# Optimization experiments

Hardware: AMD Instinct MI355X
Metric: run time of the kernel (lower is better)

The kernel has to match this reference:

```python
import jax, jax.numpy as jnp
import numpy as np

HID, HQ, HKV, D, W = 2880, 64, 8, 64, 128  # hidden, q heads, kv heads, head_dim, sliding window
SCALE = D ** -0.5
NEG = -1e30


def _rope(x, cos, sin):
    # x: [B,S,H,D]; cos/sin: [S, D//2]
    c = cos[None, :, None, :].astype(x.dtype)
    s = sin[None, :, None, :].astype(x.dtype)
    x1, x2 = jnp.split(x, 2, axis=-1)
    return jnp.concatenate([x1 * c - x2 * s, x2 * c + x1 * s], axis=-1)


def setup_inputs() -> dict:
    key = jax.random.key(0)
    ks = jax.random.split(key, 12)
    B, S = 1, 4096
    std = 0.02
    x = jax.random.normal(ks[0], (B, S, HID), jnp.float32)
    # realistic rotary table (cos || sin), half-dim each
    inv_freq = 1.0 / (150000.0 ** (np.arange(0, D, 2, dtype=np.float32) / D))
    ang = np.arange(S, dtype=np.float32)[:, None] * inv_freq[None, :]
    freqs_cis = jnp.asarray(np.concatenate([np.cos(ang), np.sin(ang)], axis=-1), jnp.float32)  # [S, D]
    Wq = jax.random.normal(ks[1], (HID, HQ * D), jnp.float32) * std
    bq = jnp.zeros((HQ * D,), jnp.float32)
    Wk = jax.random.normal(ks[2], (HID, HKV * D), jnp.float32) * std
    bk = jnp.zeros((HKV * D,), jnp.float32)
    Wv = jax.random.normal(ks[3], (HID, HKV * D), jnp.float32) * std
    bv = jnp.zeros((HKV * D,), jnp.float32)
    Wo = jax.random.normal(ks[4], (HQ * D, HID), jnp.float32) * std
    bo = jnp.zeros((HID,), jnp.float32)
    sinks = jax.random.normal(ks[5], (HQ,), jnp.float32) * std
    return {"x": x, "freqs_cis": freqs_cis, "Wq": Wq, "bq": bq, "Wk": Wk, "bk": bk,
            "Wv": Wv, "bv": bv, "Wo": Wo, "bo": bo, "sinks": sinks}


def reference(x, freqs_cis, Wq, bq, Wk, bk, Wv, bv, Wo, bo, sinks):
    B, S, _ = x.shape
    G = HQ // HKV
    nb = S // W  # S must be a multiple of W
    cos, sin = jnp.split(freqs_cis, 2, axis=-1)

    q = (x @ Wq + bq).reshape(B, S, HQ, D)
    k = (x @ Wk + bk).reshape(B, S, HKV, D)
    v = (x @ Wv + bv).reshape(B, S, HKV, D)
    q = _rope(q, cos, sin)
    k = _rope(k, cos, sin)

    q = q.transpose(0, 2, 1, 3)  # [B,HQ,S,D]
    k = k.transpose(0, 2, 1, 3)  # [B,HKV,S,D]
    v = v.transpose(0, 2, 1, 3)

    # blocked sliding-window: each query block of size W sees keys [blk*W - W, blk*W + W)
    qb = q.reshape(B, HKV, G, nb, W, D)
    kp = jnp.pad(k, ((0, 0), (0, 0), (W, 0), (0, 0)))  # prepend W zero keys
    vp = jnp.pad(v, ((0, 0), (0, 0), (W, 0), (0, 0)))
    widx = jnp.arange(nb)[:, None] * W + jnp.arange(2 * W)[None, :]  # [nb, 2W]
    kb = kp[:, :, widx]  # [B,HKV,nb,2W,D]
    vb = vp[:, :, widx]

    scores = jnp.einsum('bkgntd,bkncd->bkgntc', qb, kb) * SCALE  # [B,HKV,G,nb,W,2W]

    t = jnp.arange(W)[:, None]
    j = jnp.arange(2 * W)[None, :]
    band = (j >= t + 1) & (j <= t + W)  # 0 <= qpos - kpos <= W-1
    kpos_ok = (jnp.arange(nb)[:, None] * W - W + jnp.arange(2 * W)[None, :]) >= 0  # [nb,2W]
    mask = band[None, :, :] & kpos_ok[:, None, :]  # [nb,W,2W]
    scores = jnp.where(mask[None, None, None], scores, NEG)

    sink = sinks.reshape(HKV, G)[None, :, :, None, None]  # [1,HKV,G,1,1]
    m = jnp.maximum(scores.max(axis=-1), sink)  # [B,HKV,G,nb,W]
    e = jnp.exp(scores - m[..., None])
    denom = e.sum(axis=-1) + jnp.exp(sink - m)
    p = e / denom[..., None]

    o = jnp.einsum('bkgntc,bkncd->bkgntd', p, vb)  # [B,HKV,G,nb,W,D]
    o = o.reshape(B, HQ, S, D).transpose(0, 2, 1, 3).reshape(B, S, HQ * D)
    return o @ Wo + bo
```

## Files before the change

### kernel.cpp

```cpp
#include <hip/hip_runtime.h>
#include <hip/hip_bf16.h>
#include <stdint.h>


typedef __attribute__((ext_vector_type(8))) short bf16x8;
typedef __attribute__((ext_vector_type(4))) float f32x4;
typedef __attribute__((ext_vector_type(8))) unsigned short ushort8;

#define DEVI static __device__ __forceinline__

DEVI unsigned short f2bf(float f) {
  unsigned x = __float_as_uint(f);
  return (unsigned short)((x + 0x7fffu + ((x >> 16) & 1u)) >> 16);
}
DEVI float bf2f(unsigned short u) { return __uint_as_float(((unsigned)u) << 16); }

DEVI void async16(const void* g, void* l) {
  __builtin_amdgcn_global_load_lds(
      (const __attribute__((address_space(1))) void*)g,
      (__attribute__((address_space(3))) void*)l, 16, 0, 0);
}

__global__ void k_cast_bf16(const float* __restrict__ src,
                            unsigned short* __restrict__ dst, long n) {
  long i = ((long)blockIdx.x * blockDim.x + threadIdx.x) * 4;
  const long stride = (long)gridDim.x * blockDim.x * 4;
  for (; i < n; i += stride) {
    float4 v = *(const float4*)(src + i);
    ushort4 o = make_ushort4(f2bf(v.x), f2bf(v.y), f2bf(v.z), f2bf(v.w));
    *(ushort4*)(dst + i) = o;
  }
}

__global__ void k_transpose_cast(const float* __restrict__ src,
                                 unsigned short* __restrict__ dst,
                                 int R, int C) {
  __shared__ float tile[64][65];
  const int t = threadIdx.x;
  const int r0 = blockIdx.y * 64, c0 = blockIdx.x * 64;
#pragma unroll
  for (int i = 0; i < 16; i++) {
    int r = i * 4 + (t >> 6), c = t & 63;
    float v = 0.f;
    if (c0 + c < C) v = src[(long)(r0 + r) * C + c0 + c];
    tile[r][c] = v;
  }
  __syncthreads();
#pragma unroll
  for (int i = 0; i < 16; i++) {
    int nn = i * 4 + (t >> 6), kk = t & 63;
    dst[(long)(c0 + nn) * R + r0 + kk] = f2bf(tile[kk][nn]);
  }
}

__global__ void k_concat_bias(const float* __restrict__ bq,
                              const float* __restrict__ bk,
                              const float* __restrict__ bv,
                              float* __restrict__ dst) {
  int i = blockIdx.x * 256 + threadIdx.x;
  if (i < 5120)
    dst[i] = (i < 4096) ? bq[i] : ((i < 4608) ? bk[i - 4096] : bv[i - 4608]);
}

#define STG(c, half, t)                                                        \
  do {                                                                         \
    const int tt_ = ((t) < NT) ? (t) : NT - 1;                                 \
    const long ko_ = (long)tt_ * 64;                                           \
    if ((half) < 2) {                                                          \
      const unsigned short* s_ = gA + (long)(half) * 128 * Kd + ko_;           \
      unsigned short* d_ = &As_[c][(((half) * 128) + w8) * 64];                \
      async16(s_, d_);                                                         \
      async16(s_ + 64 * (long)Kd, d_ + 64 * 64);                               \
    } else {                                                                   \
      const unsigned short* s_ = gB + (long)((half) - 2) * 128 * Kd + ko_;     \
      unsigned short* d_ = &Bs_[c][((((half) - 2) * 128) + w8) * 64];          \
      async16(s_, d_);                                                         \
      async16(s_ + 64 * (long)Kd, d_ + 64 * 64);                               \
    }                                                                          \
  } while (0)

#define LOADA(c, mh)                                                           \
  do {                                                                         \
    _Pragma("unroll") for (int m4 = 0; m4 < 4; m4++) {                         \
      const unsigned short* r_ =                                               \
          &As_[c][(wr128 + ((mh)*4 + m4) * 16 + ll) * 64];                     \
      aF[m4][0] = *(const bf16x8*)(r_ + sl0 * 8);                              \
      aF[m4][1] = *(const bf16x8*)(r_ + sl1 * 8);                              \
    }                                                                          \
  } while (0)

#define LOADB(c, nh)                                                           \
  do {                                                                         \
    _Pragma("unroll") for (int n2 = 0; n2 < 2; n2++) {                         \
      const unsigned short* r_ =                                               \
          &Bs_[c][(wc64 + ((nh)*2 + n2) * 16 + ll) * 64];                      \
      bF[nh][n2][0] = *(const bf16x8*)(r_ + sl0 * 8);                          \
      bF[nh][n2][1] = *(const bf16x8*)(r_ + sl1 * 8);                          \
    }                                                                          \
  } while (0)

#define MFMAQ(mh, nh)                                                          \
  do {                                                                         \
    __builtin_amdgcn_s_setprio(1);                                             \
    _Pragma("unroll") for (int m4 = 0; m4 < 4; m4++)                           \
        _Pragma("unroll") for (int n2 = 0; n2 < 2; n2++) {                     \
      acc[(mh)*4 + m4][(nh)*2 + n2] = __builtin_amdgcn_mfma_f32_16x16x32_bf16( \
          aF[m4][0], bF[nh][n2][0], acc[(mh)*4 + m4][(nh)*2 + n2], 0, 0, 0);   \
      acc[(mh)*4 + m4][(nh)*2 + n2] = __builtin_amdgcn_mfma_f32_16x16x32_bf16( \
          aF[m4][1], bF[nh][n2][1], acc[(mh)*4 + m4][(nh)*2 + n2], 0, 0, 0);   \
    }                                                                          \
    __builtin_amdgcn_s_setprio(0);                                             \
  } while (0)

#define BAR() __builtin_amdgcn_s_barrier()
#define VM2() asm volatile("s_waitcnt vmcnt(2)" ::: "memory")

template <bool OUT_BF16, bool NMASK>
__global__ __launch_bounds__(512, 2) void k_gemm8(
    const unsigned short* __restrict__ A, const unsigned short* __restrict__ Bt,
    const float* __restrict__ bias, void* __restrict__ Cout,
    int Kd, int NN, int ldc, int Nreal) {
  __shared__ unsigned short As_[2][256 * 64];
  __shared__ unsigned short Bs_[2][256 * 64];
  const int tid = threadIdx.x;
  const int w = tid >> 6, l = tid & 63;
  const int wr = w >> 2, wc = w & 3;
  const int lg = l >> 4, ll = l & 15;
  const int w8 = w * 8;
  const int wr128 = wr * 128, wc64 = wc * 64;
  const int sl0 = lg ^ (ll & 7), sl1 = sl0 ^ 4;
  const int NT = Kd >> 6;

  const int b = blockIdx.x;
  const int cpx = gridDim.x >> 3;
  const int tile = (b & 7) * cpx + (b >> 3);
  const int tm = tile / NN, tn = tile % NN;
  const long m0 = (long)tm * 256, n0 = (long)tn * 256;

  const unsigned short* gA =
      A + (m0 + (tid >> 3)) * (long)Kd + (((tid & 7) ^ ((tid >> 3) & 7)) << 3);
  const unsigned short* gB =
      Bt + (n0 + (tid >> 3)) * (long)Kd + (((tid & 7) ^ ((tid >> 3) & 7)) << 3);

  f32x4 acc[8][4];
#pragma unroll
  for (int i = 0; i < 8; i++)
#pragma unroll
    for (int j = 0; j < 4; j++) acc[i][j] = (f32x4){0.f, 0.f, 0.f, 0.f};
  bf16x8 aF[4][2], bF[2][2][2];

  STG(0, 0, 0); STG(0, 1, 0); STG(0, 2, 0); STG(0, 3, 0);
  STG(1, 0, 1);
  VM2();
  BAR();

  const int NITER = NT >> 1;
  for (int i = 0; i < NITER; i++) {
    const int t = 2 * i;
    LOADA(0, 0); LOADB(0, 0); STG(1, 1, t + 1); BAR(); MFMAQ(0, 0); BAR();
    LOADB(0, 1);              STG(1, 2, t + 1); BAR(); MFMAQ(0, 1); BAR();
    LOADA(0, 1);              STG(1, 3, t + 1); BAR(); MFMAQ(1, 1); BAR();
    STG(0, 0, t + 2); VM2();                    BAR(); MFMAQ(1, 0); BAR();
    LOADA(1, 0); LOADB(1, 0); STG(0, 1, t + 2); BAR(); MFMAQ(0, 0); BAR();
    LOADB(1, 1);              STG(0, 2, t + 2); BAR(); MFMAQ(0, 1); BAR();
    LOADA(1, 1);              STG(0, 3, t + 2); BAR(); MFMAQ(1, 1); BAR();
    STG(1, 0, t + 3); VM2();                    BAR(); MFMAQ(1, 0); BAR();
  }
  if (NT & 1) {
    LOADA(0, 0); LOADB(0, 0); MFMAQ(0, 0);
    LOADB(0, 1); MFMAQ(0, 1);
    LOADA(0, 1); MFMAQ(1, 1);
    MFMAQ(1, 0);
  }

#pragma unroll
  for (int nn = 0; nn < 4; nn++) {
    int col = (int)n0 + wc64 + nn * 16 + ll;
    bool ok = (!NMASK) || (col < Nreal);
    float bv_ = ok ? bias[col] : 0.f;
#pragma unroll
    for (int m = 0; m < 8; m++) {
      long row = m0 + wr128 + m * 16 + lg * 4;
#pragma unroll
      for (int j = 0; j < 4; j++) {
        float v = acc[m][nn][j] + bv_;
        if (ok) {
          if (OUT_BF16)
            ((unsigned short*)Cout)[(row + j) * (long)ldc + col] = f2bf(v);
          else
            ((float*)Cout)[(row + j) * (long)ldc + col] = v;
        }
      }
    }
  }
}

__global__ void k_rope(unsigned short* __restrict__ qkv,
                       const float* __restrict__ fc) {
  const int s = blockIdx.x;
  const float* f = fc + (long)s * 64;
  unsigned short* row = qkv + (long)s * 5120;
  for (int i = threadIdx.x; i < 72 * 32; i += 256) {
    int hh = i >> 5, d = i & 31;
    float c = f[d], sn = f[32 + d];
    int base = hh * 64 + d;
    float x1 = bf2f(row[base]), x2 = bf2f(row[base + 32]);
    row[base] = f2bf(x1 * c - x2 * sn);
    row[base + 32] = f2bf(x2 * c + x1 * sn);
  }
}

__global__ void k_transpose_v(const unsigned short* __restrict__ qkv,
                              unsigned short* __restrict__ vt) {
  __shared__ unsigned short tile[64][72];
  const int t = threadIdx.x;
  const int ts = blockIdx.x;
  const int tj = blockIdx.y;
#pragma unroll
  for (int i = 0; i < 2; i++) {
    int s = i * 32 + (t >> 3), j = (t & 7) * 8;
    *(ushort8*)&tile[s][j] =
        *(const ushort8*)(qkv + (long)(ts * 64 + s) * 5120 + 4608 + tj * 64 + j);
  }
  __syncthreads();
  int j = t >> 2, s0 = (t & 3) * 16;
  ushort8 v0, v1;
#pragma unroll
  for (int x = 0; x < 8; x++) {
    v0[x] = tile[s0 + x][j];
    v1[x] = tile[s0 + 8 + x][j];
  }
  unsigned short* dst = vt + (long)(tj * 64 + j) * 4096 + ts * 64 + s0;
  *(ushort8*)dst = v0;
  *(ushort8*)(dst + 8) = v1;
}

__global__ __launch_bounds__(256) void k_attn(
    const unsigned short* __restrict__ qkv, const unsigned short* __restrict__ vt,
    const float* __restrict__ sinks, unsigned short* __restrict__ o) {
  __shared__ unsigned short Ps[4][32][136];
  __shared__ unsigned short Ks[128][72];
  __shared__ unsigned short Vts[64][136];
  unsigned short(*Qs)[72] = (unsigned short(*)[72]) & Ps[0][0][0];

  const int n = blockIdx.x, h = blockIdx.y;
  const int kvh = h >> 3;
  const int t = threadIdx.x, w = t >> 6, l = t & 63;
  const int lg = l >> 4, ll = l & 15;

#pragma unroll
  for (int i = 0; i < 4; i++) {
    int s = 32 * i + (t >> 3), c8 = (t & 7) * 8;
    *(ushort8*)&Qs[s][c8] =
        *(const ushort8*)(qkv + (long)(n * 128 + s) * 5120 + h * 64 + c8);
  }
  __syncthreads();
  bf16x8 aq[2][2];
#pragma unroll
  for (int m = 0; m < 2; m++)
#pragma unroll
    for (int ks = 0; ks < 2; ks++)
      aq[m][ks] = *(const bf16x8*)&Qs[32 * w + 16 * m + ll][32 * ks + 8 * lg];

  f32x4 oacc[2][4];
#pragma unroll
  for (int m = 0; m < 2; m++)
#pragma unroll
    for (int nt = 0; nt < 4; nt++) oacc[m][nt] = (f32x4){0.f, 0.f, 0.f, 0.f};
  float mrun[2][4], lrun[2][4];
#pragma unroll
  for (int m = 0; m < 2; m++)
#pragma unroll
    for (int j = 0; j < 4; j++) { mrun[m][j] = -3.0e38f; lrun[m][j] = 0.f; }

  for (int ch = (n == 0 ? 1 : 0); ch < 2; ch++) {
    const int kbase = (n - 1 + ch) * 128;
#pragma unroll
    for (int i = 0; i < 4; i++) {
      int c = 32 * i + (t >> 3), c8 = (t & 7) * 8;
      *(ushort8*)&Ks[c][c8] = *(const ushort8*)(
          qkv + (long)(kbase + c) * 5120 + 4096 + kvh * 64 + c8);
    }
#pragma unroll
    for (int i = 0; i < 4; i++) {
      int d = 16 * i + (t >> 4), c8 = (t & 15) * 8;
      *(ushort8*)&Vts[d][c8] =
          *(const ushort8*)(vt + (long)(kvh * 64 + d) * 4096 + kbase + c8);
    }
    __syncthreads();

    f32x4 sacc[2][8];
#pragma unroll
    for (int m = 0; m < 2; m++)
#pragma unroll
      for (int ct = 0; ct < 8; ct++) sacc[m][ct] = (f32x4){0.f, 0.f, 0.f, 0.f};
#pragma unroll
    for (int ct = 0; ct < 8; ct++)
#pragma unroll
      for (int ks = 0; ks < 2; ks++) {
        bf16x8 bk = *(const bf16x8*)&Ks[16 * ct + ll][32 * ks + 8 * lg];
#pragma unroll
        for (int m = 0; m < 2; m++)
          sacc[m][ct] = __builtin_amdgcn_mfma_f32_16x16x32_bf16(
              aq[m][ks], bk, sacc[m][ct], 0, 0, 0);
      }

    float cmax[2][4];
#pragma unroll
    for (int m = 0; m < 2; m++)
#pragma unroll
      for (int j = 0; j < 4; j++) cmax[m][j] = -3.0e38f;
#pragma unroll
    for (int m = 0; m < 2; m++)
#pragma unroll
      for (int ct = 0; ct < 8; ct++)
#pragma unroll
        for (int j = 0; j < 4; j++) {
          int trow = 32 * w + 16 * m + 4 * lg + j;
          int cc = ch * 128 + 16 * ct + ll;
          bool valid = (cc >= trow + 1) && (cc <= trow + 128);
          float sv = valid ? sacc[m][ct][j] * 0.125f : -1.0e30f;
          sacc[m][ct][j] = sv;
          cmax[m][j] = fmaxf(cmax[m][j], sv);
        }
#pragma unroll
    for (int m = 0; m < 2; m++)
#pragma unroll
      for (int j = 0; j < 4; j++) {
        float v = cmax[m][j];
#pragma unroll
        for (int off = 1; off < 16; off <<= 1) v = fmaxf(v, __shfl_xor(v, off));
        cmax[m][j] = v;
      }

    float fsc[2][4];
#pragma unroll
    for (int m = 0; m < 2; m++)
#pragma unroll
      for (int j = 0; j < 4; j++) {
        float mnew = fmaxf(mrun[m][j], cmax[m][j]);
        fsc[m][j] = __expf(mrun[m][j] - mnew);
        mrun[m][j] = mnew;
        lrun[m][j] *= fsc[m][j];
      }

    float psum[2][4];
#pragma unroll
    for (int m = 0; m < 2; m++)
#pragma unroll
      for (int j = 0; j < 4; j++) psum[m][j] = 0.f;
#pragma unroll
    for (int m = 0; m < 2; m++)
#pragma unroll
      for (int ct = 0; ct < 8; ct++)
#pragma unroll
        for (int j = 0; j < 4; j++) {
          float p = __expf(sacc[m][ct][j] - mrun[m][j]);
          psum[m][j] += p;
          Ps[w][16 * m + 4 * lg + j][16 * ct + ll] = f2bf(p);
        }
#pragma unroll
    for (int m = 0; m < 2; m++)
#pragma unroll
      for (int j = 0; j < 4; j++) {
        float v = psum[m][j];
#pragma unroll
        for (int off = 1; off < 16; off <<= 1) v += __shfl_xor(v, off);
        lrun[m][j] += v;
#pragma unroll
        for (int nt = 0; nt < 4; nt++) oacc[m][nt][j] *= fsc[m][j];
      }

    asm volatile("s_waitcnt lgkmcnt(0)" ::: "memory");

#pragma unroll
    for (int ks = 0; ks < 4; ks++) {
      bf16x8 pa[2], vb[4];
#pragma unroll
      for (int m = 0; m < 2; m++)
        pa[m] = *(const bf16x8*)&Ps[w][16 * m + ll][32 * ks + 8 * lg];
#pragma unroll
      for (int nt = 0; nt < 4; nt++)
        vb[nt] = *(const bf16x8*)&Vts[16 * nt + ll][32 * ks + 8 * lg];
#pragma unroll
      for (int m = 0; m < 2; m++)
#pragma unroll
        for (int nt = 0; nt < 4; nt++)
          oacc[m][nt] = __builtin_amdgcn_mfma_f32_16x16x32_bf16(
              pa[m], vb[nt], oacc[m][nt], 0, 0, 0);
    }
    __syncthreads();
  }

  const float sk = sinks[h];
#pragma unroll
  for (int m = 0; m < 2; m++)
#pragma unroll
    for (int j = 0; j < 4; j++) {
      float mf = fmaxf(mrun[m][j], sk);
      float f = __expf(mrun[m][j] - mf);
      float denom = lrun[m][j] * f + __expf(sk - mf);
      float sc = f / denom;
#pragma unroll
      for (int nt = 0; nt < 4; nt++) oacc[m][nt][j] *= sc;
    }
#pragma unroll
  for (int m = 0; m < 2; m++)
#pragma unroll
    for (int nt = 0; nt < 4; nt++)
#pragma unroll
      for (int j = 0; j < 4; j++) {
        long row = (long)n * 128 + 32 * w + 16 * m + 4 * lg + j;
        int col = h * 64 + 16 * nt + ll;
        o[row * 4096 + col] = f2bf(oacc[m][nt][j]);
      }
}

extern "C" void kernel_launch(void* const* d_in, const int* in_sizes, int n_in,
                              void* d_out, int out_size, void* d_ws,
                              size_t ws_size, hipStream_t stream) {
  const float* x = (const float*)d_in[0];
  const float* fc = (const float*)d_in[1];
  const float* Wq = (const float*)d_in[2];
  const float* bq = (const float*)d_in[3];
  const float* Wk = (const float*)d_in[4];
  const float* bk = (const float*)d_in[5];
  const float* Wv = (const float*)d_in[6];
  const float* bv = (const float*)d_in[7];
  const float* Wo = (const float*)d_in[8];
  const float* bo = (const float*)d_in[9];
  const float* sinks = (const float*)d_in[10];
  float* out = (float*)d_out;

  char* p = (char*)d_ws;
  unsigned short* xb = (unsigned short*)p;
  unsigned short* obuf = (unsigned short*)p;
  p += (size_t)4096 * 2880 * 2;
  unsigned short* Wqkvt = (unsigned short*)p;  p += (size_t)5120 * 2880 * 2;
  unsigned short* Wot = (unsigned short*)p;    p += (size_t)3072 * 4096 * 2;
  unsigned short* qkv = (unsigned short*)p;    p += (size_t)4096 * 5120 * 2;
  unsigned short* vt = (unsigned short*)p;     p += (size_t)512 * 4096 * 2;
  float* biasq = (float*)p;                    p += (size_t)5120 * 4;

  k_cast_bf16<<<2048, 256, 0, stream>>>(x, xb, (long)4096 * 2880);
  k_transpose_cast<<<dim3(64, 45), 256, 0, stream>>>(Wq, Wqkvt, 2880, 4096);
  k_transpose_cast<<<dim3(8, 45), 256, 0, stream>>>(
      Wk, Wqkvt + (size_t)4096 * 2880, 2880, 512);
  k_transpose_cast<<<dim3(8, 45), 256, 0, stream>>>(
      Wv, Wqkvt + (size_t)4608 * 2880, 2880, 512);
  k_transpose_cast<<<dim3(48, 64), 256, 0, stream>>>(Wo, Wot, 4096, 2880);
  k_concat_bias<<<20, 256, 0, stream>>>(bq, bk, bv, biasq);

  k_gemm8<true, false><<<16 * 20, 512, 0, stream>>>(
      xb, Wqkvt, biasq, qkv, 2880, 20, 5120, 5120);

  k_rope<<<4096, 256, 0, stream>>>(qkv, fc);
  k_transpose_v<<<dim3(64, 8), 256, 0, stream>>>(qkv, vt);

  k_attn<<<dim3(32, 64), 256, 0, stream>>>(qkv, vt, sinks, obuf);

  k_gemm8<false, true><<<16 * 12, 512, 0, stream>>>(
      obuf, Wot, bo, out, 4096, 12, 2880, 2880);
}
```

Measured before the change: 654.7 us.

## Skip masked attention tiles, vectorize RoPE, remap GEMM tiles, move vmcnt wait

The attention kernel now skips QK^T MFMAs, softmax work and PV MFMAs for 16-wide key tiles that the sliding-window band fully masks for each wave. This removes roughly half of the attention compute, and the chunk loop is unrolled so those conditions become compile-time. The GEMM block-to-tile mapping becomes a 2D grouped layout per XCD for better L2 reuse, and the vmcnt wait moves after the last MFMA quarter to overlap the loads. RoPE now processes 8 elements per thread with 16-byte loads and stores, at the cost of extra launch threads and some divergence.

```diff
diff --git a/kernel.cpp b/kernel.cpp
--- a/kernel.cpp
+++ b/kernel.cpp
@@ -119,7 +119,7 @@
 __global__ __launch_bounds__(512, 2) void k_gemm8(
     const unsigned short* __restrict__ A, const unsigned short* __restrict__ Bt,
     const float* __restrict__ bias, void* __restrict__ Cout,
-    int Kd, int NN, int ldc, int Nreal) {
+    int Kd, int TMX, int TNX, int ldc, int Nreal) {
   __shared__ unsigned short As_[2][256 * 64];
   __shared__ unsigned short Bs_[2][256 * 64];
   const int tid = threadIdx.x;
@@ -132,9 +132,9 @@
   const int NT = Kd >> 6;
 
   const int b = blockIdx.x;
-  const int cpx = gridDim.x >> 3;
-  const int tile = (b & 7) * cpx + (b >> 3);
-  const int tm = tile / NN, tn = tile % NN;
+  const int x = b & 7, r = b >> 3;
+  const int tm = (x >> 1) * TMX + (r % TMX);
+  const int tn = (x & 1) * TNX + (r / TMX);
   const long m0 = (long)tm * 256, n0 = (long)tn * 256;
 
   const unsigned short* gA =
@@ -160,11 +160,11 @@
     LOADA(0, 0); LOADB(0, 0); STG(1, 1, t + 1); BAR(); MFMAQ(0, 0); BAR();
     LOADB(0, 1);              STG(1, 2, t + 1); BAR(); MFMAQ(0, 1); BAR();
     LOADA(0, 1);              STG(1, 3, t + 1); BAR(); MFMAQ(1, 1); BAR();
-    STG(0, 0, t + 2); VM2();                    BAR(); MFMAQ(1, 0); BAR();
+    STG(0, 0, t + 2);                           BAR(); MFMAQ(1, 0); VM2(); BAR();
     LOADA(1, 0); LOADB(1, 0); STG(0, 1, t + 2); BAR(); MFMAQ(0, 0); BAR();
     LOADB(1, 1);              STG(0, 2, t + 2); BAR(); MFMAQ(0, 1); BAR();
     LOADA(1, 1);              STG(0, 3, t + 2); BAR(); MFMAQ(1, 1); BAR();
-    STG(1, 0, t + 3); VM2();                    BAR(); MFMAQ(1, 0); BAR();
+    STG(1, 0, t + 3);                           BAR(); MFMAQ(1, 0); VM2(); BAR();
   }
   if (NT & 1) {
     LOADA(0, 0); LOADB(0, 0); MFMAQ(0, 0);
@@ -200,13 +200,21 @@
   const int s = blockIdx.x;
   const float* f = fc + (long)s * 64;
   unsigned short* row = qkv + (long)s * 5120;
-  for (int i = threadIdx.x; i < 72 * 32; i += 256) {
-    int hh = i >> 5, d = i & 31;
-    float c = f[d], sn = f[32 + d];
-    int base = hh * 64 + d;
-    float x1 = bf2f(row[base]), x2 = bf2f(row[base + 32]);
-    row[base] = f2bf(x1 * c - x2 * sn);
-    row[base + 32] = f2bf(x2 * c + x1 * sn);
+  const int i = threadIdx.x;
+  if (i < 288) {
+    const int hh = i >> 2, g = (i & 3) * 8;
+    ushort8 a = *(const ushort8*)&row[hh * 64 + g];
+    ushort8 b = *(const ushort8*)&row[hh * 64 + 32 + g];
+    ushort8 ra, rb;
+#pragma unroll
+    for (int e = 0; e < 8; e++) {
+      float c = f[g + e], sn = f[32 + g + e];
+      float x1 = bf2f(a[e]), x2 = bf2f(b[e]);
+      ra[e] = f2bf(x1 * c - x2 * sn);
+      rb[e] = f2bf(x2 * c + x1 * sn);
+    }
+    *(ushort8*)&row[hh * 64 + g] = ra;
+    *(ushort8*)&row[hh * 64 + 32 + g] = rb;
   }
 }
 
@@ -247,6 +255,7 @@
   const int kvh = h >> 3;
   const int t = threadIdx.x, w = t >> 6, l = t & 63;
   const int lg = l >> 4, ll = l & 15;
+  const int w2 = 2 * w;
 
 #pragma unroll
   for (int i = 0; i < 4; i++) {
@@ -273,7 +282,9 @@
 #pragma unroll
     for (int j = 0; j < 4; j++) { mrun[m][j] = -3.0e38f; lrun[m][j] = 0.f; }
 
-  for (int ch = (n == 0 ? 1 : 0); ch < 2; ch++) {
+#pragma unroll
+  for (int ch = 0; ch < 2; ch++) {
+    if (ch == 0 && n == 0) continue;
     const int kbase = (n - 1 + ch) * 128;
 #pragma unroll
     for (int i = 0; i < 4; i++) {
@@ -295,15 +306,22 @@
 #pragma unroll
       for (int ct = 0; ct < 8; ct++) sacc[m][ct] = (f32x4){0.f, 0.f, 0.f, 0.f};
 #pragma unroll
-    for (int ct = 0; ct < 8; ct++)
-#pragma unroll
-      for (int ks = 0; ks < 2; ks++) {
-        bf16x8 bk = *(const bf16x8*)&Ks[16 * ct + ll][32 * ks + 8 * lg];
-#pragma unroll
-        for (int m = 0; m < 2; m++)
+    for (int ct = 0; ct < 8; ct++) {
+      const bool pvkeep = (ch == 0) ? (ct >= w2) : (ct <= w2 + 1);
+      if (!pvkeep) continue;
+      bf16x8 bk0 = *(const bf16x8*)&Ks[16 * ct + ll][8 * lg];
+      bf16x8 bk1 = *(const bf16x8*)&Ks[16 * ct + ll][32 + 8 * lg];
+#pragma unroll
+      for (int m = 0; m < 2; m++) {
+        const bool qkv_ok = (ch == 0) ? (ct >= w2 + m) : (ct <= w2 + m);
+        if (qkv_ok) {
           sacc[m][ct] = __builtin_amdgcn_mfma_f32_16x16x32_bf16(
-              aq[m][ks], bk, sacc[m][ct], 0, 0, 0);
-      }
+              aq[m][0], bk0, sacc[m][ct], 0, 0, 0);
+          sacc[m][ct] = __builtin_amdgcn_mfma_f32_16x16x32_bf16(
+              aq[m][1], bk1, sacc[m][ct], 0, 0, 0);
+        }
+      }
+    }
 
     float cmax[2][4];
 #pragma unroll
@@ -313,7 +331,9 @@
 #pragma unroll
     for (int m = 0; m < 2; m++)
 #pragma unroll
-      for (int ct = 0; ct < 8; ct++)
+      for (int ct = 0; ct < 8; ct++) {
+        const bool pvkeep = (ch == 0) ? (ct >= w2) : (ct <= w2 + 1);
+        if (!pvkeep) continue;
 #pragma unroll
         for (int j = 0; j < 4; j++) {
           int trow = 32 * w + 16 * m + 4 * lg + j;
@@ -323,6 +343,7 @@
           sacc[m][ct][j] = sv;
           cmax[m][j] = fmaxf(cmax[m][j], sv);
         }
+      }
 #pragma unroll
     for (int m = 0; m < 2; m++)
 #pragma unroll
@@ -352,13 +373,16 @@
 #pragma unroll
     for (int m = 0; m < 2; m++)
 #pragma unroll
-      for (int ct = 0; ct < 8; ct++)
+      for (int ct = 0; ct < 8; ct++) {
+        const bool pvkeep = (ch == 0) ? (ct >= w2) : (ct <= w2 + 1);
+        if (!pvkeep) continue;
 #pragma unroll
         for (int j = 0; j < 4; j++) {
           float p = __expf(sacc[m][ct][j] - mrun[m][j]);
           psum[m][j] += p;
           Ps[w][16 * m + 4 * lg + j][16 * ct + ll] = f2bf(p);
         }
+      }
 #pragma unroll
     for (int m = 0; m < 2; m++)
 #pragma unroll
@@ -375,6 +399,8 @@
 
 #pragma unroll
     for (int ks = 0; ks < 4; ks++) {
+      const bool keep = (ch == 0) ? (ks >= w) : (ks <= w);
+      if (!keep) continue;
       bf16x8 pa[2], vb[4];
 #pragma unroll
       for (int m = 0; m < 2; m++)
@@ -451,14 +477,14 @@
   k_transpose_cast<<<dim3(48, 64), 256, 0, stream>>>(Wo, Wot, 4096, 2880);
   k_concat_bias<<<20, 256, 0, stream>>>(bq, bk, bv, biasq);
 
-  k_gemm8<true, false><<<16 * 20, 512, 0, stream>>>(
-      xb, Wqkvt, biasq, qkv, 2880, 20, 5120, 5120);
-
-  k_rope<<<4096, 256, 0, stream>>>(qkv, fc);
+  k_gemm8<true, false><<<320, 512, 0, stream>>>(
+      xb, Wqkvt, biasq, qkv, 2880, 4, 10, 5120, 5120);
+
+  k_rope<<<4096, 320, 0, stream>>>(qkv, fc);
   k_transpose_v<<<dim3(64, 8), 256, 0, stream>>>(qkv, vt);
 
   k_attn<<<dim3(32, 64), 256, 0, stream>>>(qkv, vt, sinks, obuf);
 
-  k_gemm8<false, true><<<16 * 12, 512, 0, stream>>>(
-      obuf, Wot, bo, out, 4096, 12, 2880, 2880);
-}
+  k_gemm8<false, true><<<192, 512, 0, stream>>>(
+      obuf, Wot, bo, out, 4096, 4, 6, 2880, 2880);
+}
```

After: 584.8 us. 10.7% less time.
